# Kernel optimization log

Measured on AMD Instinct MI355X. Metric: run time of the kernel, lower is better.

The kernel has to match this reference:

```python
import jax, jax.numpy as jnp
import numpy as np

N_NODES = 100000
N_EDGES = 3200000
C, H, F = 512, 256, 64


def spmm(edge_row, edge_col, edge_val, Z):
    # (A @ Z)[i] = sum over edges e with row[e]==i of val[e] * Z[col[e]]
    msgs = edge_val[:, None] * Z[edge_col]  # [E, d]
    return jax.ops.segment_sum(msgs, edge_row, num_segments=N_NODES)


def setup_inputs() -> dict:
    key = jax.random.key(0)
    k1, k2, k3, k4, k5, k6, k7 = jax.random.split(key, 7)
    X = jax.random.normal(k1, (N_NODES, C), dtype=jnp.float32)
    edge_row = jax.random.randint(k2, (N_EDGES,), 0, N_NODES, dtype=jnp.int32)
    edge_col = jax.random.randint(k3, (N_EDGES,), 0, N_NODES, dtype=jnp.int32)
    edge_val = jax.random.uniform(k4, (N_EDGES,), dtype=jnp.float32)
    W0 = jax.random.normal(k5, (C, H), dtype=jnp.float32) * (C ** -0.5)
    Wh1 = jax.random.normal(k6, (H, H), dtype=jnp.float32) * (H ** -0.5)
    W1 = jax.random.normal(k7, (H, F), dtype=jnp.float32) * (H ** -0.5)
    return {"X": X, "edge_row": edge_row, "edge_col": edge_col,
            "edge_val": edge_val, "W0": W0, "Wh1": Wh1, "W1": W1}


def reference(X, edge_row, edge_col, edge_val, W0, Wh1, W1):
    # layer 0: relu(A @ (X W0))   (dropout=0 -> identity)
    Z = jax.nn.relu(spmm(edge_row, edge_col, edge_val, X @ W0))
    # hidden layers (num_layers - 2 = 1)
    Z = jax.nn.relu(spmm(edge_row, edge_col, edge_val, Z @ Wh1))
    # output layer: softmax(A @ (Z W1), axis=-1)
    Z = jax.nn.softmax(spmm(edge_row, edge_col, edge_val, Z @ W1), axis=-1)
    return Z
```

## Files before the change

### kernel.cpp

```cpp
#include <hip/hip_runtime.h>
#include <cstdint>
#include <cstddef>


#define SCAN_B 1024

typedef __attribute__((ext_vector_type(8))) short short8_t;
typedef __attribute__((ext_vector_type(4))) short short4_t;
typedef __attribute__((ext_vector_type(4))) float f32x4;

__device__ __forceinline__ short bf16_hi(float x) {
    union { float f; unsigned u; } c; c.f = x;
    return (short)(c.u >> 16);
}
__device__ __forceinline__ float bf16_f32(short h) {
    union { float f; unsigned u; } c; c.u = ((unsigned)(unsigned short)h) << 16;
    return c.f;
}

__device__ __forceinline__ void gload_lds16(const void* g, void* l) {
    __builtin_amdgcn_global_load_lds(
        (const __attribute__((address_space(1))) void*)g,
        (__attribute__((address_space(3))) void*)l, 16, 0, 0);
}


__global__ void count_rows_k(const int* __restrict__ row, int* __restrict__ deg, int E) {
    int e = blockIdx.x * blockDim.x + threadIdx.x;
    if (e < E) atomicAdd(&deg[row[e]], 1);
}

__global__ __launch_bounds__(SCAN_B) void scan1_k(const int* __restrict__ deg,
                                                  int* __restrict__ part,
                                                  int* __restrict__ bsum, int n) {
    __shared__ int buf[SCAN_B];
    int tid = threadIdx.x;
    int i = blockIdx.x * SCAN_B + tid;
    int v = (i < n) ? ((deg[i] + 3) & ~3) : 0;
    buf[tid] = v;
    __syncthreads();
    for (int off = 1; off < SCAN_B; off <<= 1) {
        int y = (tid >= off) ? buf[tid - off] : 0;
        __syncthreads();
        buf[tid] += y;
        __syncthreads();
    }
    if (i < n) part[i] = buf[tid] - v;
    if (tid == SCAN_B - 1) bsum[blockIdx.x] = buf[tid];
}

__global__ __launch_bounds__(128) void scan2_k(int* __restrict__ bsum, int nb) {
    __shared__ int buf[128];
    int tid = threadIdx.x;
    int v = (tid < nb) ? bsum[tid] : 0;
    buf[tid] = v;
    __syncthreads();
    for (int off = 1; off < 128; off <<= 1) {
        int y = (tid >= off) ? buf[tid - off] : 0;
        __syncthreads();
        buf[tid] += y;
        __syncthreads();
    }
    if (tid < nb) bsum[tid] = buf[tid] - v;
    if (tid == nb - 1) bsum[nb] = buf[tid];
}

__global__ __launch_bounds__(SCAN_B) void scan3_k(int* __restrict__ rowptr,
                                                  const int* __restrict__ bsum,
                                                  int* __restrict__ cursor, int n, int nb) {
    int i = blockIdx.x * SCAN_B + threadIdx.x;
    if (i < n) {
        int v = rowptr[i] + bsum[blockIdx.x];
        rowptr[i] = v;
        cursor[i] = v;
    }
    if (i == 0) rowptr[n] = bsum[nb];
}

__global__ void scatter_k(const int* __restrict__ row, const int* __restrict__ col,
                          const float* __restrict__ val, int* __restrict__ cursor,
                          int* __restrict__ scol, float* __restrict__ sval, int E) {
    int e = blockIdx.x * blockDim.x + threadIdx.x;
    if (e < E) {
        int r = row[e];
        int p = atomicAdd(&cursor[r], 1);
        scol[p] = col[e];
        sval[p] = val[e];
    }
}


__global__ void split_w_k(const float* __restrict__ W, short* __restrict__ Bhl,
                          int K, int M) {
    int i = blockIdx.x * 256 + threadIdx.x;
    if (i >= K * M) return;
    int k = i / M, m = i - k * M;
    float x = W[i];
    short hi = bf16_hi(x);
    float r = x - bf16_f32(hi);
    short lo = bf16_hi(r);
    int g = k >> 3, j = k & 7;
    Bhl[(size_t)m * (2 * K) + 16 * g + j] = hi;
    Bhl[(size_t)m * (2 * K) + 16 * g + 8 + j] = lo;
}


template <int K, int BN, int NWC>
__global__ __launch_bounds__(256) void gemm_fq(const float* __restrict__ A,
                                               const short* __restrict__ Bhl,
                                               short* __restrict__ ZQ,
                                               float* __restrict__ scl, int N) {
    constexpr int NWR = 4 / NWC;
    constexpr int BM  = 32 * NWR;
    constexpr int NF  = BN / NWC / 16;
    __shared__ float Ald[BM * 32];
    __shared__ short Bld[BN * 64];

    const int tid = threadIdx.x, lane = tid & 63, w = tid >> 6;
    const int wr = w / NWC, wc = w % NWC;
    const int row0 = blockIdx.x * BM;
    const int l8 = lane >> 3;
    const int slotx = (lane & 7) ^ (l8 & 7);
    const bool full = (row0 + BM <= N);

    f32x4 acc[2][NF] = {};

    for (int k0 = 0; k0 < K; k0 += 32) {
        if (full) {
            for (int ch = w; ch < BM / 8; ch += 4)
                gload_lds16(A + (size_t)(row0 + ch * 8 + l8) * K + k0 + slotx * 4,
                            &Ald[ch * 256]);
        } else {
            for (int ch = w; ch < BM / 8; ch += 4) {
                int r_ = row0 + ch * 8 + l8;
                float4 v = make_float4(0.f, 0.f, 0.f, 0.f);
                if (r_ < N) v = *(const float4*)(A + (size_t)r_ * K + k0 + slotx * 4);
                *(float4*)((char*)&Ald[ch * 256] + lane * 16) = v;
            }
        }
        for (int ch = w; ch < BN / 8; ch += 4)
            gload_lds16(Bhl + (size_t)(ch * 8 + l8) * (2 * K) + 2 * k0 + slotx * 8,
                        &Bld[ch * 512]);
        __syncthreads();

        const int g2 = (lane >> 4) * 2;
        short8_t ah[2], al[2];
#pragma unroll
        for (int m = 0; m < 2; ++m) {
            int rl = wr * 32 + m * 16 + (lane & 15);
            int key = rl & 7;
            f32x4 a0 = *(const f32x4*)&Ald[rl * 32 + ((g2 ^ key) * 4)];
            f32x4 a1 = *(const f32x4*)&Ald[rl * 32 + (((g2 + 1) ^ key) * 4)];
            float f[8] = {a0[0], a0[1], a0[2], a0[3], a1[0], a1[1], a1[2], a1[3]};
#pragma unroll
            for (int j = 0; j < 8; ++j) {
                short hh = bf16_hi(f[j]);
                ah[m][j] = hh;
                al[m][j] = bf16_hi(f[j] - bf16_f32(hh));
            }
        }
#pragma unroll
        for (int n = 0; n < NF; ++n) {
            int cl = wc * (BN / NWC) + n * 16 + (lane & 15);
            int key = cl & 7;
            short8_t bh = *(const short8_t*)&Bld[cl * 64 + ((g2 ^ key) * 8)];
            short8_t bl = *(const short8_t*)&Bld[cl * 64 + (((g2 + 1) ^ key) * 8)];
#pragma unroll
            for (int m = 0; m < 2; ++m) {
                acc[m][n] = __builtin_amdgcn_mfma_f32_16x16x32_bf16(ah[m], bh, acc[m][n], 0, 0, 0);
                acc[m][n] = __builtin_amdgcn_mfma_f32_16x16x32_bf16(ah[m], bl, acc[m][n], 0, 0, 0);
                acc[m][n] = __builtin_amdgcn_mfma_f32_16x16x32_bf16(al[m], bh, acc[m][n], 0, 0, 0);
            }
        }
        __syncthreads();
    }

    const int lg = lane >> 4, lc = lane & 15;
    float* maxb = Ald;
    float rmax[2][4];
#pragma unroll
    for (int m = 0; m < 2; ++m)
#pragma unroll
        for (int r = 0; r < 4; ++r) {
            float v = 0.f;
#pragma unroll
            for (int n = 0; n < NF; ++n) v = fmaxf(v, fabsf(acc[m][n][r]));
#pragma unroll
            for (int o = 8; o >= 1; o >>= 1) v = fmaxf(v, __shfl_xor(v, o));
            rmax[m][r] = v;
        }
    if constexpr (NWC > 1) {
        if (lc == 0)
#pragma unroll
            for (int m = 0; m < 2; ++m)
#pragma unroll
                for (int r = 0; r < 4; ++r)
                    maxb[(wr * 32 + m * 16 + lg * 4 + r) * NWC + wc] = rmax[m][r];
        __syncthreads();
    }
#pragma unroll
    for (int m = 0; m < 2; ++m)
#pragma unroll
        for (int r = 0; r < 4; ++r) {
            int rl = wr * 32 + m * 16 + lg * 4 + r;
            float v = rmax[m][r];
            if constexpr (NWC > 1) {
                v = maxb[rl * NWC];
#pragma unroll
                for (int q = 1; q < NWC; ++q) v = fmaxf(v, maxb[rl * NWC + q]);
            }
            int grow = row0 + rl;
            if (grow < N) {
                float inv = (v > 0.f) ? 32767.f / v : 0.f;
                if (lc == 0 && wc == 0) scl[grow] = v * (1.f / 32767.f);
#pragma unroll
                for (int n = 0; n < NF; ++n)
                    ZQ[(size_t)grow * BN + wc * (BN / NWC) + n * 16 + lc] =
                        (short)rintf(acc[m][n][r] * inv);
            }
        }
}


__global__ __launch_bounds__(256) void spmm_agg256_k(const int* __restrict__ rowptr,
                                                     const int* __restrict__ scol,
                                                     const float* __restrict__ sval,
                                                     const short* __restrict__ Q,
                                                     const float* __restrict__ scl,
                                                     float* __restrict__ Z, int N) {
    int row = blockIdx.x * 4 + (threadIdx.x >> 6);
    if (row >= N) return;
    int lane = threadIdx.x & 63;
    int s = rowptr[row], e = rowptr[row + 1];
    const short4_t* Qv = (const short4_t*)Q;
    f32x4 acc = {0.f, 0.f, 0.f, 0.f};
    for (int i = s; i < e; i += 4) {
        int4 c4 = *(const int4*)&scol[i];
        float4 v4 = *(const float4*)&sval[i];
        float w0 = v4.x * scl[c4.x];
        float w1 = v4.y * scl[c4.y];
        float w2 = v4.z * scl[c4.z];
        float w3 = v4.w * scl[c4.w];
        short4_t q0 = Qv[(size_t)c4.x * 64 + lane];
        short4_t q1 = Qv[(size_t)c4.y * 64 + lane];
        short4_t q2 = Qv[(size_t)c4.z * 64 + lane];
        short4_t q3 = Qv[(size_t)c4.w * 64 + lane];
#pragma unroll
        for (int j = 0; j < 4; ++j) {
            acc[j] = fmaf(w0, (float)q0[j], acc[j]);
            acc[j] = fmaf(w1, (float)q1[j], acc[j]);
            acc[j] = fmaf(w2, (float)q2[j], acc[j]);
            acc[j] = fmaf(w3, (float)q3[j], acc[j]);
        }
    }
    float4 out = make_float4(fmaxf(acc[0], 0.f), fmaxf(acc[1], 0.f),
                             fmaxf(acc[2], 0.f), fmaxf(acc[3], 0.f));
    ((float4*)Z)[(size_t)row * 64 + lane] = out;
}

__global__ __launch_bounds__(256) void spmm_softmax64_k(const int* __restrict__ rowptr,
                                                        const int* __restrict__ scol,
                                                        const float* __restrict__ sval,
                                                        const short* __restrict__ Q,
                                                        const float* __restrict__ scl,
                                                        float* __restrict__ out, int N) {
    int row = blockIdx.x * 4 + (threadIdx.x >> 6);
    if (row >= N) return;
    int lane = threadIdx.x & 63;
    int s = rowptr[row], e = rowptr[row + 1];
    float acc = 0.f;
    for (int i = s; i < e; i += 4) {
        int4 c4 = *(const int4*)&scol[i];
        float4 v4 = *(const float4*)&sval[i];
        float w0 = v4.x * scl[c4.x];
        float w1 = v4.y * scl[c4.y];
        float w2 = v4.z * scl[c4.z];
        float w3 = v4.w * scl[c4.w];
        float z0 = (float)Q[(size_t)c4.x * 64 + lane];
        float z1 = (float)Q[(size_t)c4.y * 64 + lane];
        float z2 = (float)Q[(size_t)c4.z * 64 + lane];
        float z3 = (float)Q[(size_t)c4.w * 64 + lane];
        acc = fmaf(w0, z0, acc);
        acc = fmaf(w1, z1, acc);
        acc = fmaf(w2, z2, acc);
        acc = fmaf(w3, z3, acc);
    }
    float m = acc;
#pragma unroll
    for (int o = 32; o >= 1; o >>= 1) m = fmaxf(m, __shfl_xor(m, o));
    float p = __expf(acc - m);
    float ssum = p;
#pragma unroll
    for (int o = 32; o >= 1; o >>= 1) ssum += __shfl_xor(ssum, o);
    out[(size_t)row * 64 + lane] = p / ssum;
}


extern "C" void kernel_launch(void* const* d_in, const int* in_sizes, int n_in,
                              void* d_out, int out_size, void* d_ws, size_t ws_size,
                              hipStream_t stream) {
    const float* X        = (const float*)d_in[0];
    const int*   edge_row = (const int*)d_in[1];
    const int*   edge_col = (const int*)d_in[2];
    const float* edge_val = (const float*)d_in[3];
    const float* W0       = (const float*)d_in[4];
    const float* Wh1      = (const float*)d_in[5];
    const float* W1       = (const float*)d_in[6];

    const int C = 512, H = 256, F = 64;
    const int N = in_sizes[0] / C;
    const int E = in_sizes[1];
    const int EPAD = E + 4 * N + 64;

    size_t off = 0;
    auto alloc = [&](size_t bytes) -> void* {
        void* p = (char*)d_ws + off;
        off += (bytes + 255) & ~(size_t)255;
        return p;
    };
    float* Z      = (float*)alloc((size_t)N * H * sizeof(float));
    short* ZQ     = (short*)alloc((size_t)N * H * sizeof(short));
    float* scl    = (float*)alloc((size_t)N * sizeof(float));
    int*   deg    = (int*)alloc((size_t)N * sizeof(int));
    int*   rowptr = (int*)alloc((size_t)(N + 1) * sizeof(int));
    int*   cursor = (int*)alloc((size_t)N * sizeof(int));
    int*   bsum   = (int*)alloc(129 * sizeof(int));
    int*   scol   = (int*)alloc((size_t)EPAD * sizeof(int));
    float* sval   = (float*)alloc((size_t)EPAD * sizeof(float));
    short* Bhl0   = (short*)alloc((size_t)H * 2 * C * sizeof(short));
    short* Bhl1   = (short*)alloc((size_t)H * 2 * H * sizeof(short));
    short* Bhl2   = (short*)alloc((size_t)F * 2 * H * sizeof(short));
    (void)ws_size;

    hipMemsetAsync(deg, 0, (size_t)N * sizeof(int), stream);
    hipMemsetAsync(scol, 0, (size_t)EPAD * sizeof(int), stream);
    hipMemsetAsync(sval, 0, (size_t)EPAD * sizeof(float), stream);
    count_rows_k<<<(E + 255) / 256, 256, 0, stream>>>(edge_row, deg, E);
    int nb = (N + SCAN_B - 1) / SCAN_B;
    scan1_k<<<nb, SCAN_B, 0, stream>>>(deg, rowptr, bsum, N);
    scan2_k<<<1, 128, 0, stream>>>(bsum, nb);
    scan3_k<<<nb, SCAN_B, 0, stream>>>(rowptr, bsum, cursor, N, nb);
    scatter_k<<<(E + 255) / 256, 256, 0, stream>>>(edge_row, edge_col, edge_val,
                                                   cursor, scol, sval, E);

    split_w_k<<<(C * H + 255) / 256, 256, 0, stream>>>(W0, Bhl0, C, H);
    split_w_k<<<(H * H + 255) / 256, 256, 0, stream>>>(Wh1, Bhl1, H, H);
    split_w_k<<<(H * F + 255) / 256, 256, 0, stream>>>(W1, Bhl2, H, F);

    const int g64  = (N + 63) / 64;
    const int g128 = (N + 127) / 128;
    const int rg   = (N + 3) / 4;

    gemm_fq<512, 256, 2><<<g64, 256, 0, stream>>>(X, Bhl0, ZQ, scl, N);
    spmm_agg256_k<<<rg, 256, 0, stream>>>(rowptr, scol, sval, ZQ, scl, Z, N);
    gemm_fq<256, 256, 2><<<g64, 256, 0, stream>>>(Z, Bhl1, ZQ, scl, N);
    spmm_agg256_k<<<rg, 256, 0, stream>>>(rowptr, scol, sval, ZQ, scl, Z, N);
    gemm_fq<256, 64, 1><<<g128, 256, 0, stream>>>(Z, Bhl2, ZQ, scl, N);
    spmm_softmax64_k<<<rg, 256, 0, stream>>>(rowptr, scol, sval, ZQ, scl,
                                             (float*)d_out, N);
}
```

Baseline: 1.161 ms.

## Emit bf16 hi/lo split from SpMM, interleave edge col/val, reshape GEMM tiles

The SpMM aggregation kernels now write the ReLU output directly as interleaved bf16 hi/lo pairs in the layout the next GEMM loads. That GEMM then streams A straight into LDS and no longer converts fp32 to hi/lo inside every tile. Edge column indices and values are packed into one int2 array, so the gather loop issues one load stream instead of two. The GEMM is reworked so each wave covers 64 rows with four M fragments, using a 1x4 or 2x2 wave grid. The first layer does its fp32-to-hi/lo split once while staging tiles into LDS. This trades more registers and a larger Zhl buffer for less conversion ALU work and less intermediate traffic.

```diff
diff --git a/kernel.cpp b/kernel.cpp
--- a/kernel.cpp
+++ b/kernel.cpp
@@ -79,13 +79,12 @@
 
 __global__ void scatter_k(const int* __restrict__ row, const int* __restrict__ col,
                           const float* __restrict__ val, int* __restrict__ cursor,
-                          int* __restrict__ scol, float* __restrict__ sval, int E) {
+                          int2* __restrict__ ecv, int E) {
     int e = blockIdx.x * blockDim.x + threadIdx.x;
     if (e < E) {
         int r = row[e];
         int p = atomicAdd(&cursor[r], 1);
-        scol[p] = col[e];
-        sval[p] = val[e];
+        ecv[p] = make_int2(col[e], __float_as_int(val[e]));
     }
 }
 
@@ -105,68 +104,73 @@
 }
 
 
-template <int K, int BN, int NWC>
-__global__ __launch_bounds__(256) void gemm_fq(const float* __restrict__ A,
+template <int K, int BN, int NWR, int NWC, bool AF32>
+__global__ __launch_bounds__(256) void gemm_hl(const void* __restrict__ Av,
                                                const short* __restrict__ Bhl,
                                                short* __restrict__ ZQ,
                                                float* __restrict__ scl, int N) {
-    constexpr int NWR = 4 / NWC;
-    constexpr int BM  = 32 * NWR;
-    constexpr int NF  = BN / NWC / 16;
-    __shared__ float Ald[BM * 32];
+    constexpr int BM = 64 * NWR;
+    constexpr int NF = BN / NWC / 16;
+    __shared__ short Ald[BM * 64];
     __shared__ short Bld[BN * 64];
 
     const int tid = threadIdx.x, lane = tid & 63, w = tid >> 6;
     const int wr = w / NWC, wc = w % NWC;
     const int row0 = blockIdx.x * BM;
     const int l8 = lane >> 3;
-    const int slotx = (lane & 7) ^ (l8 & 7);
-    const bool full = (row0 + BM <= N);
-
-    f32x4 acc[2][NF] = {};
+    const int sx = (lane & 7) ^ l8;
+
+    f32x4 acc[4][NF] = {};
 
     for (int k0 = 0; k0 < K; k0 += 32) {
-        if (full) {
-            for (int ch = w; ch < BM / 8; ch += 4)
-                gload_lds16(A + (size_t)(row0 + ch * 8 + l8) * K + k0 + slotx * 4,
-                            &Ald[ch * 256]);
-        } else {
-            for (int ch = w; ch < BM / 8; ch += 4) {
-                int r_ = row0 + ch * 8 + l8;
-                float4 v = make_float4(0.f, 0.f, 0.f, 0.f);
-                if (r_ < N) v = *(const float4*)(A + (size_t)r_ * K + k0 + slotx * 4);
-                *(float4*)((char*)&Ald[ch * 256] + lane * 16) = v;
-            }
-        }
-        for (int ch = w; ch < BN / 8; ch += 4)
-            gload_lds16(Bhl + (size_t)(ch * 8 + l8) * (2 * K) + 2 * k0 + slotx * 8,
-                        &Bld[ch * 512]);
-        __syncthreads();
-
-        const int g2 = (lane >> 4) * 2;
-        short8_t ah[2], al[2];
-#pragma unroll
-        for (int m = 0; m < 2; ++m) {
-            int rl = wr * 32 + m * 16 + (lane & 15);
-            int key = rl & 7;
-            f32x4 a0 = *(const f32x4*)&Ald[rl * 32 + ((g2 ^ key) * 4)];
-            f32x4 a1 = *(const f32x4*)&Ald[rl * 32 + (((g2 + 1) ^ key) * 4)];
-            float f[8] = {a0[0], a0[1], a0[2], a0[3], a1[0], a1[1], a1[2], a1[3]};
+        if constexpr (AF32) {
+            const float* A = (const float*)Av;
+            int row = tid >> 2, q = tid & 3;
+            int gr = row0 + row;
+            float4 x0 = make_float4(0.f, 0.f, 0.f, 0.f), x1 = x0;
+            if (gr < N) {
+                x0 = *(const float4*)&A[(size_t)gr * K + k0 + q * 8];
+                x1 = *(const float4*)&A[(size_t)gr * K + k0 + q * 8 + 4];
+            }
+            float f[8] = {x0.x, x0.y, x0.z, x0.w, x1.x, x1.y, x1.z, x1.w};
+            short8_t hi, lo;
 #pragma unroll
             for (int j = 0; j < 8; ++j) {
                 short hh = bf16_hi(f[j]);
-                ah[m][j] = hh;
-                al[m][j] = bf16_hi(f[j] - bf16_f32(hh));
-            }
+                hi[j] = hh;
+                lo[j] = bf16_hi(f[j] - bf16_f32(hh));
+            }
+            int key = row & 7;
+            *(short8_t*)&Ald[row * 64 + ((2 * q) ^ key) * 8] = hi;
+            *(short8_t*)&Ald[row * 64 + ((2 * q + 1) ^ key) * 8] = lo;
+        } else {
+            const short* Ahl = (const short*)Av;
+            for (int ch = w; ch < BM / 8; ch += 4)
+                gload_lds16(Ahl + (size_t)(row0 + ch * 8 + l8) * (2 * K) + 2 * k0 + sx * 8,
+                            &Ald[ch * 512]);
+        }
+        for (int ch = w; ch < BN / 8; ch += 4)
+            gload_lds16(Bhl + (size_t)(ch * 8 + l8) * (2 * K) + 2 * k0 + sx * 8,
+                        &Bld[ch * 512]);
+        __syncthreads();
+
+        const int sH = (lane >> 4) * 2, sL = sH + 1;
+        short8_t ah[4], al[4];
+#pragma unroll
+        for (int m = 0; m < 4; ++m) {
+            int rl = wr * 64 + m * 16 + (lane & 15);
+            int key = rl & 7;
+            ah[m] = *(const short8_t*)&Ald[rl * 64 + (sH ^ key) * 8];
+            al[m] = *(const short8_t*)&Ald[rl * 64 + (sL ^ key) * 8];
         }
 #pragma unroll
         for (int n = 0; n < NF; ++n) {
             int cl = wc * (BN / NWC) + n * 16 + (lane & 15);
             int key = cl & 7;
-            short8_t bh = *(const short8_t*)&Bld[cl * 64 + ((g2 ^ key) * 8)];
-            short8_t bl = *(const short8_t*)&Bld[cl * 64 + (((g2 + 1) ^ key) * 8)];
-#pragma unroll
-            for (int m = 0; m < 2; ++m) {
+            short8_t bh = *(const short8_t*)&Bld[cl * 64 + (sH ^ key) * 8];
+            short8_t bl = *(const short8_t*)&Bld[cl * 64 + (sL ^ key) * 8];
+#pragma unroll
+            for (int m = 0; m < 4; ++m) {
                 acc[m][n] = __builtin_amdgcn_mfma_f32_16x16x32_bf16(ah[m], bh, acc[m][n], 0, 0, 0);
                 acc[m][n] = __builtin_amdgcn_mfma_f32_16x16x32_bf16(ah[m], bl, acc[m][n], 0, 0, 0);
                 acc[m][n] = __builtin_amdgcn_mfma_f32_16x16x32_bf16(al[m], bh, acc[m][n], 0, 0, 0);
@@ -176,10 +180,10 @@
     }
 
     const int lg = lane >> 4, lc = lane & 15;
-    float* maxb = Ald;
-    float rmax[2][4];
-#pragma unroll
-    for (int m = 0; m < 2; ++m)
+    float* maxb = (float*)Ald;
+    float rmax[4][4];
+#pragma unroll
+    for (int m = 0; m < 4; ++m)
 #pragma unroll
         for (int r = 0; r < 4; ++r) {
             float v = 0.f;
@@ -192,17 +196,17 @@
     if constexpr (NWC > 1) {
         if (lc == 0)
 #pragma unroll
-            for (int m = 0; m < 2; ++m)
+            for (int m = 0; m < 4; ++m)
 #pragma unroll
                 for (int r = 0; r < 4; ++r)
-                    maxb[(wr * 32 + m * 16 + lg * 4 + r) * NWC + wc] = rmax[m][r];
-        __syncthreads();
-    }
-#pragma unroll
-    for (int m = 0; m < 2; ++m)
+                    maxb[(wr * 64 + m * 16 + lg * 4 + r) * NWC + wc] = rmax[m][r];
+        __syncthreads();
+    }
+#pragma unroll
+    for (int m = 0; m < 4; ++m)
 #pragma unroll
         for (int r = 0; r < 4; ++r) {
-            int rl = wr * 32 + m * 16 + lg * 4 + r;
+            int rl = wr * 64 + m * 16 + lg * 4 + r;
             float v = rmax[m][r];
             if constexpr (NWC > 1) {
                 v = maxb[rl * NWC];
@@ -223,11 +227,10 @@
 
 
 __global__ __launch_bounds__(256) void spmm_agg256_k(const int* __restrict__ rowptr,
-                                                     const int* __restrict__ scol,
-                                                     const float* __restrict__ sval,
+                                                     const int2* __restrict__ ecv,
                                                      const short* __restrict__ Q,
                                                      const float* __restrict__ scl,
-                                                     float* __restrict__ Z, int N) {
+                                                     short* __restrict__ Zhl, int N) {
     int row = blockIdx.x * 4 + (threadIdx.x >> 6);
     if (row >= N) return;
     int lane = threadIdx.x & 63;
@@ -235,16 +238,16 @@
     const short4_t* Qv = (const short4_t*)Q;
     f32x4 acc = {0.f, 0.f, 0.f, 0.f};
     for (int i = s; i < e; i += 4) {
-        int4 c4 = *(const int4*)&scol[i];
-        float4 v4 = *(const float4*)&sval[i];
-        float w0 = v4.x * scl[c4.x];
-        float w1 = v4.y * scl[c4.y];
-        float w2 = v4.z * scl[c4.z];
-        float w3 = v4.w * scl[c4.w];
-        short4_t q0 = Qv[(size_t)c4.x * 64 + lane];
-        short4_t q1 = Qv[(size_t)c4.y * 64 + lane];
-        short4_t q2 = Qv[(size_t)c4.z * 64 + lane];
-        short4_t q3 = Qv[(size_t)c4.w * 64 + lane];
+        int4 a = *(const int4*)(ecv + i);
+        int4 b = *(const int4*)(ecv + i + 2);
+        float w0 = __int_as_float(a.y) * scl[a.x];
+        float w1 = __int_as_float(a.w) * scl[a.z];
+        float w2 = __int_as_float(b.y) * scl[b.x];
+        float w3 = __int_as_float(b.w) * scl[b.z];
+        short4_t q0 = Qv[(size_t)a.x * 64 + lane];
+        short4_t q1 = Qv[(size_t)a.z * 64 + lane];
+        short4_t q2 = Qv[(size_t)b.x * 64 + lane];
+        short4_t q3 = Qv[(size_t)b.z * 64 + lane];
 #pragma unroll
         for (int j = 0; j < 4; ++j) {
             acc[j] = fmaf(w0, (float)q0[j], acc[j]);
@@ -253,14 +256,21 @@
             acc[j] = fmaf(w3, (float)q3[j], acc[j]);
         }
     }
-    float4 out = make_float4(fmaxf(acc[0], 0.f), fmaxf(acc[1], 0.f),
-                             fmaxf(acc[2], 0.f), fmaxf(acc[3], 0.f));
-    ((float4*)Z)[(size_t)row * 64 + lane] = out;
+    short4_t hi, lo;
+#pragma unroll
+    for (int j = 0; j < 4; ++j) {
+        float r = fmaxf(acc[j], 0.f);
+        short h = bf16_hi(r);
+        hi[j] = h;
+        lo[j] = bf16_hi(r - bf16_f32(h));
+    }
+    size_t base = (size_t)row * 512 + (lane >> 1) * 16 + (lane & 1) * 4;
+    *(short4_t*)&Zhl[base] = hi;
+    *(short4_t*)&Zhl[base + 8] = lo;
 }
 
 __global__ __launch_bounds__(256) void spmm_softmax64_k(const int* __restrict__ rowptr,
-                                                        const int* __restrict__ scol,
-                                                        const float* __restrict__ sval,
+                                                        const int2* __restrict__ ecv,
                                                         const short* __restrict__ Q,
                                                         const float* __restrict__ scl,
                                                         float* __restrict__ out, int N) {
@@ -270,16 +280,16 @@
     int s = rowptr[row], e = rowptr[row + 1];
     float acc = 0.f;
     for (int i = s; i < e; i += 4) {
-        int4 c4 = *(const int4*)&scol[i];
-        float4 v4 = *(const float4*)&sval[i];
-        float w0 = v4.x * scl[c4.x];
-        float w1 = v4.y * scl[c4.y];
-        float w2 = v4.z * scl[c4.z];
-        float w3 = v4.w * scl[c4.w];
-        float z0 = (float)Q[(size_t)c4.x * 64 + lane];
-        float z1 = (float)Q[(size_t)c4.y * 64 + lane];
-        float z2 = (float)Q[(size_t)c4.z * 64 + lane];
-        float z3 = (float)Q[(size_t)c4.w * 64 + lane];
+        int4 a = *(const int4*)(ecv + i);
+        int4 b = *(const int4*)(ecv + i + 2);
+        float w0 = __int_as_float(a.y) * scl[a.x];
+        float w1 = __int_as_float(a.w) * scl[a.z];
+        float w2 = __int_as_float(b.y) * scl[b.x];
+        float w3 = __int_as_float(b.w) * scl[b.z];
+        float z0 = (float)Q[(size_t)a.x * 64 + lane];
+        float z1 = (float)Q[(size_t)a.z * 64 + lane];
+        float z2 = (float)Q[(size_t)b.x * 64 + lane];
+        float z3 = (float)Q[(size_t)b.z * 64 + lane];
         acc = fmaf(w0, z0, acc);
         acc = fmaf(w1, z1, acc);
         acc = fmaf(w2, z2, acc);
@@ -318,30 +328,28 @@
         off += (bytes + 255) & ~(size_t)255;
         return p;
     };
-    float* Z      = (float*)alloc((size_t)N * H * sizeof(float));
+    short* Zhl    = (short*)alloc((size_t)N * 2 * H * sizeof(short));
     short* ZQ     = (short*)alloc((size_t)N * H * sizeof(short));
     float* scl    = (float*)alloc((size_t)N * sizeof(float));
     int*   deg    = (int*)alloc((size_t)N * sizeof(int));
     int*   rowptr = (int*)alloc((size_t)(N + 1) * sizeof(int));
     int*   cursor = (int*)alloc((size_t)N * sizeof(int));
     int*   bsum   = (int*)alloc(129 * sizeof(int));
-    int*   scol   = (int*)alloc((size_t)EPAD * sizeof(int));
-    float* sval   = (float*)alloc((size_t)EPAD * sizeof(float));
+    int2*  ecv    = (int2*)alloc((size_t)EPAD * sizeof(int2));
     short* Bhl0   = (short*)alloc((size_t)H * 2 * C * sizeof(short));
     short* Bhl1   = (short*)alloc((size_t)H * 2 * H * sizeof(short));
     short* Bhl2   = (short*)alloc((size_t)F * 2 * H * sizeof(short));
     (void)ws_size;
 
     hipMemsetAsync(deg, 0, (size_t)N * sizeof(int), stream);
-    hipMemsetAsync(scol, 0, (size_t)EPAD * sizeof(int), stream);
-    hipMemsetAsync(sval, 0, (size_t)EPAD * sizeof(float), stream);
+    hipMemsetAsync(ecv, 0, (size_t)EPAD * sizeof(int2), stream);
     count_rows_k<<<(E + 255) / 256, 256, 0, stream>>>(edge_row, deg, E);
     int nb = (N + SCAN_B - 1) / SCAN_B;
     scan1_k<<<nb, SCAN_B, 0, stream>>>(deg, rowptr, bsum, N);
     scan2_k<<<1, 128, 0, stream>>>(bsum, nb);
     scan3_k<<<nb, SCAN_B, 0, stream>>>(rowptr, bsum, cursor, N, nb);
     scatter_k<<<(E + 255) / 256, 256, 0, stream>>>(edge_row, edge_col, edge_val,
-                                                   cursor, scol, sval, E);
+                                                   cursor, ecv, E);
 
     split_w_k<<<(C * H + 255) / 256, 256, 0, stream>>>(W0, Bhl0, C, H);
     split_w_k<<<(H * H + 255) / 256, 256, 0, stream>>>(Wh1, Bhl1, H, H);
@@ -351,11 +359,11 @@
     const int g128 = (N + 127) / 128;
     const int rg   = (N + 3) / 4;
 
-    gemm_fq<512, 256, 2><<<g64, 256, 0, stream>>>(X, Bhl0, ZQ, scl, N);
-    spmm_agg256_k<<<rg, 256, 0, stream>>>(rowptr, scol, sval, ZQ, scl, Z, N);
-    gemm_fq<256, 256, 2><<<g64, 256, 0, stream>>>(Z, Bhl1, ZQ, scl, N);
-    spmm_agg256_k<<<rg, 256, 0, stream>>>(rowptr, scol, sval, ZQ, scl, Z, N);
-    gemm_fq<256, 64, 1><<<g128, 256, 0, stream>>>(Z, Bhl2, ZQ, scl, N);
-    spmm_softmax64_k<<<rg, 256, 0, stream>>>(rowptr, scol, sval, ZQ, scl,
+    gemm_hl<512, 256, 1, 4, true><<<g64, 256, 0, stream>>>(X, Bhl0, ZQ, scl, N);
+    spmm_agg256_k<<<rg, 256, 0, stream>>>(rowptr, ecv, ZQ, scl, Zhl, N);
+    gemm_hl<256, 256, 1, 4, false><<<g64, 256, 0, stream>>>(Zhl, Bhl1, ZQ, scl, N);
+    spmm_agg256_k<<<rg, 256, 0, stream>>>(rowptr, ecv, ZQ, scl, Zhl, N);
+    gemm_hl<256, 64, 2, 2, false><<<g128, 256, 0, stream>>>(Zhl, Bhl2, ZQ, scl, N);
+    spmm_softmax64_k<<<rg, 256, 0, stream>>>(rowptr, ecv, ZQ, scl,
                                              (float*)d_out, N);
 }
```

Result: faster. 1.136 ms (-2.2%).
